# Kernel tuning notes

Measured on AMD Instinct MI355X. Metric: run time of the kernel, lower is better.

Reference implementation:

```python
import jax, jax.numpy as jnp
import numpy as np

B, S, H = 1, 1024, 2048
NH, HD = 16, 128
E, K, FI, SFI = 8, 2, 1408, 2816
EPS = 1e-6
THETA = 10000.0


def setup_inputs() -> dict:
    key = jax.random.key(0)
    ks = jax.random.split(key, 14)
    sc = 0.02
    return {
        "hidden_states": jax.random.normal(ks[0], (B, S, H), jnp.float32),
        "ln1_w": jnp.ones((H,), jnp.float32),
        "ln2_w": jnp.ones((H,), jnp.float32),
        "wq": jax.random.normal(ks[1], (H, H), jnp.float32) * sc,
        "wk": jax.random.normal(ks[2], (H, H), jnp.float32) * sc,
        "wv": jax.random.normal(ks[3], (H, H), jnp.float32) * sc,
        "wo": jax.random.normal(ks[4], (H, H), jnp.float32) * sc,
        "gate_w": jax.random.normal(ks[5], (E, H), jnp.float32) * sc,
        "expert_gate": jax.random.normal(ks[6], (E, FI, H), jnp.float32) * sc,
        "expert_up": jax.random.normal(ks[7], (E, FI, H), jnp.float32) * sc,
        "expert_down": jax.random.normal(ks[8], (E, H, FI), jnp.float32) * sc,
        "shared_gate": jax.random.normal(ks[9], (SFI, H), jnp.float32) * sc,
        "shared_up": jax.random.normal(ks[10], (SFI, H), jnp.float32) * sc,
        "shared_down": jax.random.normal(ks[11], (H, SFI), jnp.float32) * sc,
    }


def _rmsnorm(x, w):
    v = jnp.mean(x * x, axis=-1, keepdims=True)
    return x * jax.lax.rsqrt(v + EPS) * w


def _rotate_half(x):
    x1, x2 = x[..., : HD // 2], x[..., HD // 2 :]
    return jnp.concatenate((-x2, x1), axis=-1)


def _rope_cos_sin():
    inv_freq = 1.0 / (THETA ** (jnp.arange(0, HD, 2, dtype=jnp.float32) / HD))
    t = jnp.arange(S, dtype=jnp.float32)
    freqs = t[:, None] * inv_freq[None, :]          # [S, HD//2]
    emb = jnp.concatenate((freqs, freqs), axis=-1)  # [S, HD]
    return jnp.cos(emb)[None, None], jnp.sin(emb)[None, None]  # [1,1,S,HD]


def _decoder_layer(hidden_states, ln1_w, ln2_w, wq, wk, wv, wo, gate_w,
                   expert_gate, expert_up, expert_down,
                   shared_gate, shared_up, shared_down):
    # ---- self-attention ----
    residual = hidden_states
    h = _rmsnorm(hidden_states, ln1_w)
    q = (h @ wq.T).reshape(B, S, NH, HD).transpose(0, 2, 1, 3)  # [B,NH,S,HD]
    k = (h @ wk.T).reshape(B, S, NH, HD).transpose(0, 2, 1, 3)
    v = (h @ wv.T).reshape(B, S, NH, HD).transpose(0, 2, 1, 3)
    cos, sin = _rope_cos_sin()
    q = q * cos + _rotate_half(q) * sin
    k = k * cos + _rotate_half(k) * sin
    scores = jnp.einsum('bhqd,bhkd->bhqk', q, k) / jnp.sqrt(jnp.float32(HD))
    causal = jnp.tril(jnp.ones((S, S), bool))
    scores = jnp.where(causal[None, None], scores, jnp.finfo(jnp.float32).min)
    probs = jax.nn.softmax(scores, axis=-1)
    attn = jnp.einsum('bhqk,bhkd->bhqd', probs, v)
    attn = attn.transpose(0, 2, 1, 3).reshape(B, S, H)
    x = residual + attn @ wo.T

    # ---- MoE MLP ----
    residual = x
    h2 = _rmsnorm(x, ln2_w)
    flat = h2.reshape(-1, H)                       # [N,H], N=B*S
    n_tok = flat.shape[0]
    logits = flat @ gate_w.T                       # [N,E]
    gate_scores = jax.nn.softmax(logits, axis=-1)
    topk_w, topk_idx = jax.lax.top_k(gate_scores, K)
    topk_w = topk_w / (jnp.sum(topk_w, axis=-1, keepdims=True) + 1e-20)
    # dense combine weights [N,E] (zero for unrouted experts)
    combine = jnp.zeros((n_tok, E), flat.dtype).at[
        jnp.arange(n_tok)[:, None], topk_idx].add(topk_w)
    # SwiGLU per expert, dense over all experts, then weighted combine
    g = jnp.einsum('nh,efh->enf', flat, expert_gate)   # [E,N,FI]
    u = jnp.einsum('nh,efh->enf', flat, expert_up)
    act = jax.nn.silu(g) * u
    eo = jnp.einsum('enf,ehf->enh', act, expert_down)  # [E,N,H]
    routed = jnp.einsum('enh,ne->nh', eo, combine)
    # shared experts (always on)
    shared = (jax.nn.silu(flat @ shared_gate.T) * (flat @ shared_up.T)) @ shared_down.T
    return residual + (routed + shared).reshape(B, S, H)


def reference(hidden_states, ln1_w, ln2_w, wq, wk, wv, wo, gate_w,
              expert_gate, expert_up, expert_down,
              shared_gate, shared_up, shared_down):
    return _decoder_layer(hidden_states, ln1_w, ln2_w, wq, wk, wv, wo, gate_w,
                          expert_gate, expert_up, expert_down,
                          shared_gate, shared_up, shared_down)
```

## Files before the change

### kernel.cpp

```cpp
#include <hip/hip_runtime.h>
#include <hip/hip_bf16.h>


#define DI __device__ __forceinline__

typedef __attribute__((ext_vector_type(8))) short short8;
typedef __attribute__((ext_vector_type(4))) float f32x4;
using u16 = unsigned short;

struct alignas(8) U16x4 { u16 x, y, z, w; };

DI u16 f2bf(float f) {
  unsigned u = __float_as_uint(f);
  u += 0x7fffu + ((u >> 16) & 1u);
  return (u16)(u >> 16);
}
DI float bf2f(u16 h) { return __uint_as_float(((unsigned)h) << 16); }
DI unsigned pack2(float f0, float f1) {
  unsigned a = __float_as_uint(f0) + 0x8000u;
  unsigned b = __float_as_uint(f1) + 0x8000u;
  return (a >> 16) | (b & 0xffff0000u);
}

DI void gload16(const void* g, void* l) {
  __builtin_amdgcn_global_load_lds((const __attribute__((address_space(1))) void*)g,
                                   (__attribute__((address_space(3))) void*)l, 16, 0, 0);
}


__global__ __launch_bounds__(256) void k_ropetab(float* __restrict__ tab) {
  int idx = blockIdx.x * 256 + threadIdx.x;
  int s = idx >> 6, i = idx & 63;
  double inv = pow(10000.0, -(double)(2 * i) / 128.0);
  double ang = (double)s * inv;
  tab[idx * 2 + 0] = (float)cos(ang);
  tab[idx * 2 + 1] = (float)sin(ang);
}

__global__ __launch_bounds__(256) void k_rmsnorm(const float* __restrict__ in,
                                                 const float* __restrict__ w,
                                                 float* __restrict__ outf,
                                                 u16* __restrict__ outh,
                                                 u16* __restrict__ outl) {
  const int row = blockIdx.x, t = threadIdx.x;
  const float* x = in + (size_t)row * 2048;
  float4 a = *(const float4*)&x[t * 4];
  float4 b = *(const float4*)&x[1024 + t * 4];
  float ss = a.x * a.x + a.y * a.y + a.z * a.z + a.w * a.w +
             b.x * b.x + b.y * b.y + b.z * b.z + b.w * b.w;
#pragma unroll
  for (int off = 32; off; off >>= 1) ss += __shfl_xor(ss, off);
  __shared__ float red[4];
  if ((t & 63) == 0) red[t >> 6] = ss;
  __syncthreads();
  float total = red[0] + red[1] + red[2] + red[3];
  float r = 1.0f / sqrtf(total * (1.0f / 2048.0f) + 1e-6f);
  float4 wa = *(const float4*)&w[t * 4];
  float4 wb = *(const float4*)&w[1024 + t * 4];
  float va[8] = {a.x * r * wa.x, a.y * r * wa.y, a.z * r * wa.z, a.w * r * wa.w,
                 b.x * r * wb.x, b.y * r * wb.y, b.z * r * wb.z, b.w * r * wb.w};
  if (outf) {
    *(float4*)&outf[(size_t)row * 2048 + t * 4] = make_float4(va[0], va[1], va[2], va[3]);
    *(float4*)&outf[(size_t)row * 2048 + 1024 + t * 4] = make_float4(va[4], va[5], va[6], va[7]);
  }
  if (outh) {
    U16x4 ha{f2bf(va[0]), f2bf(va[1]), f2bf(va[2]), f2bf(va[3])};
    U16x4 hb{f2bf(va[4]), f2bf(va[5]), f2bf(va[6]), f2bf(va[7])};
    *(U16x4*)&outh[(size_t)row * 2048 + t * 4] = ha;
    *(U16x4*)&outh[(size_t)row * 2048 + 1024 + t * 4] = hb;
    if (outl) {
      U16x4 la{f2bf(va[0] - bf2f(ha.x)), f2bf(va[1] - bf2f(ha.y)),
               f2bf(va[2] - bf2f(ha.z)), f2bf(va[3] - bf2f(ha.w))};
      U16x4 lb{f2bf(va[4] - bf2f(hb.x)), f2bf(va[5] - bf2f(hb.y)),
               f2bf(va[6] - bf2f(hb.z)), f2bf(va[7] - bf2f(hb.w))};
      *(U16x4*)&outl[(size_t)row * 2048 + t * 4] = la;
      *(U16x4*)&outl[(size_t)row * 2048 + 1024 + t * 4] = lb;
    }
  }
}

__global__ __launch_bounds__(256) void k_splitf4(
    const float* __restrict__ s0, const float* __restrict__ s1,
    const float* __restrict__ s2, const float* __restrict__ s3,
    u16* __restrict__ h0, u16* __restrict__ h1, u16* __restrict__ h2,
    u16* __restrict__ h3, u16* __restrict__ l0, u16* __restrict__ l1,
    u16* __restrict__ l2, u16* __restrict__ l3) {
  const int which = blockIdx.x >> 12;
  const int idx = ((blockIdx.x & 4095) * 256 + threadIdx.x) * 4;
  const float* src = (which == 0) ? s0 : (which == 1) ? s1 : (which == 2) ? s2 : s3;
  u16* dh = (which == 0) ? h0 : (which == 1) ? h1 : (which == 2) ? h2 : h3;
  u16* dl = (which == 0) ? l0 : (which == 1) ? l1 : (which == 2) ? l2 : l3;
  float4 v = *(const float4*)&src[idx];
  U16x4 h{f2bf(v.x), f2bf(v.y), f2bf(v.z), f2bf(v.w)};
  U16x4 l{f2bf(v.x - bf2f(h.x)), f2bf(v.y - bf2f(h.y)),
          f2bf(v.z - bf2f(h.z)), f2bf(v.w - bf2f(h.w))};
  *(U16x4*)&dh[idx] = h;
  *(U16x4*)&dl[idx] = l;
}

__global__ __launch_bounds__(256) void k_rope(float* __restrict__ q, float* __restrict__ k,
                                              const float* __restrict__ tab) {
  int idx = blockIdx.x * 256 + threadIdx.x;
  int s = idx >> 10, rem = idx & 1023;
  int h = rem >> 6, i = rem & 63;
  size_t base = (size_t)s * 2048 + h * 128 + i;
  float c = tab[(s * 64 + i) * 2 + 0];
  float sn = tab[(s * 64 + i) * 2 + 1];
  const float qs = 0.08838834764831845f;
  float q1 = q[base], q2 = q[base + 64];
  q[base] = (q1 * c - q2 * sn) * qs;
  q[base + 64] = (q2 * c + q1 * sn) * qs;
  float k1 = k[base], k2 = k[base + 64];
  k[base] = k1 * c - k2 * sn;
  k[base + 64] = k2 * c + k1 * sn;
}

__global__ __launch_bounds__(256) void k_splitkv(
    const float* __restrict__ qf, const float* __restrict__ kf,
    const float* __restrict__ vf,
    u16* __restrict__ Qh, u16* __restrict__ Ql,
    u16* __restrict__ Kh, u16* __restrict__ Kl,
    u16* __restrict__ Vth, u16* __restrict__ Vtl) {
  int idx = (blockIdx.x * 256 + threadIdx.x) * 4;
  int s = idx >> 11, c = idx & 2047;
  float4 q4 = *(const float4*)&qf[idx];
  U16x4 qh{f2bf(q4.x), f2bf(q4.y), f2bf(q4.z), f2bf(q4.w)};
  U16x4 ql{f2bf(q4.x - bf2f(qh.x)), f2bf(q4.y - bf2f(qh.y)),
           f2bf(q4.z - bf2f(qh.z)), f2bf(q4.w - bf2f(qh.w))};
  *(U16x4*)&Qh[idx] = qh; *(U16x4*)&Ql[idx] = ql;
  float4 k4 = *(const float4*)&kf[idx];
  U16x4 kh{f2bf(k4.x), f2bf(k4.y), f2bf(k4.z), f2bf(k4.w)};
  U16x4 kl{f2bf(k4.x - bf2f(kh.x)), f2bf(k4.y - bf2f(kh.y)),
           f2bf(k4.z - bf2f(kh.z)), f2bf(k4.w - bf2f(kh.w))};
  *(U16x4*)&Kh[idx] = kh; *(U16x4*)&Kl[idx] = kl;
  float4 v4 = *(const float4*)&vf[idx];
  float vv[4] = {v4.x, v4.y, v4.z, v4.w};
#pragma unroll
  for (int i = 0; i < 4; ++i) {
    u16 hv = f2bf(vv[i]);
    u16 lv = f2bf(vv[i] - bf2f(hv));
    Vth[(size_t)(c + i) * 1024 + s] = hv;
    Vtl[(size_t)(c + i) * 1024 + s] = lv;
  }
}

DI void stage_kv(const u16* __restrict__ Khg, const u16* __restrict__ Klg,
                 const u16* __restrict__ Vhg, const u16* __restrict__ Vlg,
                 u16* lsKh, u16* lsKl, u16* lsVh, u16* lsVl,
                 int kvb, int hh, int wv, int lane) {
#pragma unroll
  for (int it = 0; it < 4; ++it) {
    const int ebase = it * 2048 + wv * 512;
    const int eo = ebase + lane * 8;
    {
      const int rr = eo >> 7, cg = (eo >> 3) & 15;
      const size_t src = (size_t)(kvb + rr) * 2048 + hh * 128 + ((cg ^ (rr & 7)) << 3);
      gload16(Khg + src, lsKh + ebase);
      gload16(Klg + src, lsKl + ebase);
    }
    {
      const int rr = eo >> 6, cg = (eo >> 3) & 7;
      const size_t src = (size_t)(hh * 128 + rr) * 1024 + kvb + ((cg ^ (rr & 7)) << 3);
      gload16(Vhg + src, lsVh + ebase);
      gload16(Vlg + src, lsVl + ebase);
    }
  }
}

__global__ __launch_bounds__(256) void k_attn_tile(
    const u16* __restrict__ Qh, const u16* __restrict__ Ql,
    const u16* __restrict__ Khg, const u16* __restrict__ Klg,
    const u16* __restrict__ Vhg, const u16* __restrict__ Vlg,
    u16* __restrict__ atth, u16* __restrict__ attl) {
  __shared__ u16 lsKh[2][8192], lsKl[2][8192], lsVh[2][8192], lsVl[2][8192];
  __shared__ u16 Plh[4][16][72], Pll[4][16][72];
  const int hh = blockIdx.y;
  const int qb = blockIdx.x * 64;
  const int tid = threadIdx.x, lane = tid & 63, wv = tid >> 6;
  const int l15 = lane & 15, grp = lane >> 4;
  u16(*plh)[72] = Plh[wv];
  u16(*pll)[72] = Pll[wv];
  const int q_glob = qb + wv * 16 + l15;
  const int tend = blockIdx.x + 1;

  short8 qfh[4], qfl[4];
  const size_t qbase = (size_t)q_glob * 2048 + hh * 128;
#pragma unroll
  for (int c = 0; c < 4; ++c) {
    qfh[c] = *(const short8*)&Qh[qbase + c * 32 + grp * 8];
    qfl[c] = *(const short8*)&Ql[qbase + c * 32 + grp * 8];
  }
  f32x4 oacc[8];
#pragma unroll
  for (int dc = 0; dc < 8; ++dc) oacc[dc] = 0.f;
  float m_run = -1e30f, l_run = 0.f;

  int cur = 0;
  stage_kv(Khg, Klg, Vhg, Vlg, lsKh[0], lsKl[0], lsVh[0], lsVl[0], 0, hh, wv, lane);
  __syncthreads();

  for (int kt = 0; kt < tend; ++kt) {
    const int kvb = kt * 64;
    if (kt + 1 < tend)
      stage_kv(Khg, Klg, Vhg, Vlg, lsKh[cur ^ 1], lsKl[cur ^ 1], lsVh[cur ^ 1],
               lsVl[cur ^ 1], kvb + 64, hh, wv, lane);
    const u16* kh = lsKh[cur];
    const u16* kl = lsKl[cur];
    const u16* vh = lsVh[cur];
    const u16* vl = lsVl[cur];

    f32x4 s4[4];
#pragma unroll
    for (int sub = 0; sub < 4; ++sub) {
      f32x4 a = {0.f, 0.f, 0.f, 0.f};
      const int kr = sub * 16 + l15;
      const int sw = kr & 7;
#pragma unroll
      for (int c = 0; c < 4; ++c) {
        const int off = kr * 128 + ((((c << 2) | grp) ^ sw) << 3);
        short8 khf = *(const short8*)&kh[off];
        short8 klf = *(const short8*)&kl[off];
        a = __builtin_amdgcn_mfma_f32_16x16x32_bf16(khf, qfh[c], a, 0, 0, 0);
        a = __builtin_amdgcn_mfma_f32_16x16x32_bf16(klf, qfh[c], a, 0, 0, 0);
        a = __builtin_amdgcn_mfma_f32_16x16x32_bf16(khf, qfl[c], a, 0, 0, 0);
      }
      s4[sub] = a;
    }
    if (kt == tend - 1) {
#pragma unroll
      for (int sub = 0; sub < 4; ++sub)
#pragma unroll
        for (int r = 0; r < 4; ++r) {
          int kv = kvb + sub * 16 + grp * 4 + r;
          if (kv > q_glob) s4[sub][r] = -1e30f;
        }
    }
    float tmax = s4[0][0];
#pragma unroll
    for (int sub = 0; sub < 4; ++sub)
#pragma unroll
      for (int r = 0; r < 4; ++r) tmax = fmaxf(tmax, s4[sub][r]);
    tmax = fmaxf(tmax, __shfl_xor(tmax, 16));
    tmax = fmaxf(tmax, __shfl_xor(tmax, 32));
    float mnew = fmaxf(m_run, tmax);
    float scale = expf(m_run - mnew);
    float p[16], lsum = 0.f;
#pragma unroll
    for (int sub = 0; sub < 4; ++sub)
#pragma unroll
      for (int r = 0; r < 4; ++r) {
        float pe = expf(s4[sub][r] - mnew);
        p[sub * 4 + r] = pe;
        lsum += pe;
      }
    lsum += __shfl_xor(lsum, 16);
    lsum += __shfl_xor(lsum, 32);
    l_run = l_run * scale + lsum;
    m_run = mnew;
#pragma unroll
    for (int dc = 0; dc < 8; ++dc) oacc[dc] *= scale;
#pragma unroll
    for (int sub = 0; sub < 4; ++sub)
#pragma unroll
      for (int rp = 0; rp < 2; ++rp) {
        int i0 = sub * 4 + rp * 2;
        u16 h0 = f2bf(p[i0]), h1 = f2bf(p[i0 + 1]);
        u16 lo0 = f2bf(p[i0] - bf2f(h0)), lo1 = f2bf(p[i0 + 1] - bf2f(h1));
        int kvoff = sub * 16 + grp * 4 + rp * 2;
        *(unsigned*)&plh[l15][kvoff] = (unsigned)h0 | ((unsigned)h1 << 16);
        *(unsigned*)&pll[l15][kvoff] = (unsigned)lo0 | ((unsigned)lo1 << 16);
      }
    short8 phf[2], plf[2];
#pragma unroll
    for (int ks = 0; ks < 2; ++ks) {
      phf[ks] = *(const short8*)&plh[l15][ks * 32 + grp * 8];
      plf[ks] = *(const short8*)&pll[l15][ks * 32 + grp * 8];
    }
#pragma unroll
    for (int dc = 0; dc < 8; ++dc) {
      const int dr = dc * 16 + l15;
      const int sw = dr & 7;
      f32x4 acc = oacc[dc];
#pragma unroll
      for (int ks = 0; ks < 2; ++ks) {
        const int voff = dr * 64 + ((((ks << 2) | grp) ^ sw) << 3);
        short8 vhf = *(const short8*)&vh[voff];
        short8 vlf = *(const short8*)&vl[voff];
        acc = __builtin_amdgcn_mfma_f32_16x16x32_bf16(vhf, phf[ks], acc, 0, 0, 0);
        acc = __builtin_amdgcn_mfma_f32_16x16x32_bf16(vlf, phf[ks], acc, 0, 0, 0);
        acc = __builtin_amdgcn_mfma_f32_16x16x32_bf16(vhf, plf[ks], acc, 0, 0, 0);
      }
      oacc[dc] = acc;
    }
    __syncthreads();
    cur ^= 1;
  }
  float inv = 1.0f / l_run;
#pragma unroll
  for (int dc = 0; dc < 8; ++dc)
#pragma unroll
    for (int rp = 0; rp < 2; ++rp) {
      float v0 = oacc[dc][rp * 2] * inv;
      float v1 = oacc[dc][rp * 2 + 1] * inv;
      u16 h0 = f2bf(v0), h1 = f2bf(v1);
      u16 lo0 = f2bf(v0 - bf2f(h0)), lo1 = f2bf(v1 - bf2f(h1));
      size_t o = (size_t)q_glob * 2048 + hh * 128 + dc * 16 + grp * 4 + rp * 2;
      *(unsigned*)&atth[o] = (unsigned)h0 | ((unsigned)h1 << 16);
      *(unsigned*)&attl[o] = (unsigned)lo0 | ((unsigned)lo1 << 16);
    }
}

__global__ __launch_bounds__(256) void k_router(const float* __restrict__ h2f,
                                                const float* __restrict__ gw,
                                                int2* __restrict__ tidx,
                                                float2* __restrict__ twgt) {
  const int tok = blockIdx.x;
  const float* hrow = h2f + (size_t)tok * 2048;
  float part[8];
#pragma unroll
  for (int e = 0; e < 8; ++e) part[e] = 0.f;
  for (int j = 0; j < 8; ++j) {
    int p = j * 256 + threadIdx.x;
    float hv = hrow[p];
#pragma unroll
    for (int e = 0; e < 8; ++e) part[e] += hv * gw[e * 2048 + p];
  }
#pragma unroll
  for (int e = 0; e < 8; ++e)
#pragma unroll
    for (int off = 32; off; off >>= 1) part[e] += __shfl_xor(part[e], off);
  __shared__ float red[4][8];
  int wv = threadIdx.x >> 6, lane = threadIdx.x & 63;
  if (lane == 0) {
#pragma unroll
    for (int e = 0; e < 8; ++e) red[wv][e] = part[e];
  }
  __syncthreads();
  if (threadIdx.x == 0) {
    float lg[8];
#pragma unroll
    for (int e = 0; e < 8; ++e) lg[e] = red[0][e] + red[1][e] + red[2][e] + red[3][e];
    float m = lg[0];
#pragma unroll
    for (int e = 1; e < 8; ++e) m = fmaxf(m, lg[e]);
    float ex[8], s = 0.f;
#pragma unroll
    for (int e = 0; e < 8; ++e) { ex[e] = expf(lg[e] - m); s += ex[e]; }
#pragma unroll
    for (int e = 0; e < 8; ++e) ex[e] /= s;
    int i1 = 0;
#pragma unroll
    for (int e = 1; e < 8; ++e) if (ex[e] > ex[i1]) i1 = e;
    int i2 = (i1 == 0) ? 1 : 0;
#pragma unroll
    for (int e = 0; e < 8; ++e) if (e != i1 && ex[e] > ex[i2]) i2 = e;
    float s2 = ex[i1] + ex[i2] + 1e-20f;
    tidx[tok] = make_int2(i1, i2);
    twgt[tok] = make_float2(ex[i1] / s2, ex[i2] / s2);
  }
}

__global__ __launch_bounds__(64) void k_scan(const int2* __restrict__ tidx,
                                             const float2* __restrict__ twgt,
                                             int* __restrict__ meta,
                                             int* __restrict__ toklist,
                                             float* __restrict__ slotw,
                                             int* __restrict__ slots) {
  const int lane = threadIdx.x;
  int base = 0;
  for (int e = 0; e < 8; ++e) {
    int cnt = 0;
    for (int c = 0; c < 16; ++c) {
      const int tok = c * 64 + lane;
      int2 my = tidx[tok];
      int f1 = (my.x == e), f2 = (my.y == e);
      int flag = f1 | f2;
      unsigned long long m = __ballot(flag);
      if (flag) {
        float2 w = twgt[tok];
        int rank = (int)__popcll(m & ((1ull << lane) - 1ull));
        int s = base + cnt + rank;
        toklist[s] = tok;
        slotw[s] = f1 ? w.x : w.y;
        slots[tok * 2 + (f1 ? 0 : 1)] = s;
      }
      cnt += (int)__popcll(m);
    }
    if (lane == 0) { meta[e] = base; meta[9 + e] = cnt; }
    const int padded = ((cnt + 127) >> 7) << 7;
    for (int s = cnt + lane; s < padded; s += 64) {
      toklist[base + s] = 0;
      slotw[base + s] = 0.f;
    }
    base += padded;
  }
  if (lane == 0) meta[8] = base;
}


DI void stageA_bf16(const u16* __restrict__ A, size_t lda, int row0, int k0,
                    u16* lsA, int tid) {
  const int lane = tid & 63, wv = tid >> 6;
#pragma unroll
  for (int it = 0; it < 2; ++it) {
    const int ebase = it * 2048 + wv * 512;
    const int eo = ebase + lane * 8;
    const int rr = eo >> 5, cc = eo & 31;
    gload16(A + (size_t)(row0 + rr) * lda + k0 + cc, lsA + ebase);
  }
}

__global__ __launch_bounds__(256) void k_gemm_bf16split(
    const u16* __restrict__ Ah, const u16* __restrict__ Al,
    const u16* __restrict__ Bh0, const u16* __restrict__ Bl0,
    const u16* __restrict__ Bh1, const u16* __restrict__ Bl1,
    const u16* __restrict__ Bh2, const u16* __restrict__ Bl2,
    float* __restrict__ C0, float* __restrict__ C1, float* __restrict__ C2,
    const float* __restrict__ resid) {
  __shared__ u16 lsAh[4096], lsAl[4096], lsBh[2048], lsBl[2048];
  const int z = blockIdx.z;
  const u16* Bh = (z == 0) ? Bh0 : (z == 1) ? Bh1 : Bh2;
  const u16* Bl = (z == 0) ? Bl0 : (z == 1) ? Bl1 : Bl2;
  float* Cm = (z == 0) ? C0 : (z == 1) ? C1 : C2;
  const int tid = threadIdx.x, lane = tid & 63, wv = tid >> 6;
  const int wr = (wv >> 1) * 64, wc = (wv & 1) * 32;
  const int fr = lane & 15, fg = lane >> 4;
  const int row0 = blockIdx.x * 128, col0 = blockIdx.y * 64;
  f32x4 acc[4][2];
#pragma unroll
  for (int i = 0; i < 4; ++i)
#pragma unroll
    for (int j = 0; j < 2; ++j) acc[i][j] = 0.f;

  for (int kt = 0; kt < 64; ++kt) {
    const int k0 = kt * 32;
    stageA_bf16(Ah, 2048, row0, k0, lsAh, tid);
    stageA_bf16(Al, 2048, row0, k0, lsAl, tid);
    {
      const int ebase = wv * 512;
      const int eo = ebase + lane * 8;
      const int rr = eo >> 5, cc = eo & 31;
      const size_t src = (size_t)(col0 + rr) * 2048 + k0 + cc;
      gload16(Bh + src, lsBh + ebase);
      gload16(Bl + src, lsBl + ebase);
    }
    __syncthreads();
    short8 ah[4], al[4], bh[2], bl[2];
#pragma unroll
    for (int mi = 0; mi < 4; ++mi) {
      const int off = (wr + mi * 16 + fr) * 32 + fg * 8;
      ah[mi] = *(const short8*)&lsAh[off];
      al[mi] = *(const short8*)&lsAl[off];
    }
#pragma unroll
    for (int ni = 0; ni < 2; ++ni) {
      const int off = (wc + ni * 16 + fr) * 32 + fg * 8;
      bh[ni] = *(const short8*)&lsBh[off];
      bl[ni] = *(const short8*)&lsBl[off];
    }
#pragma unroll
    for (int mi = 0; mi < 4; ++mi)
#pragma unroll
      for (int ni = 0; ni < 2; ++ni) {
        f32x4 c = acc[mi][ni];
        c = __builtin_amdgcn_mfma_f32_16x16x32_bf16(al[mi], bh[ni], c, 0, 0, 0);
        c = __builtin_amdgcn_mfma_f32_16x16x32_bf16(ah[mi], bl[ni], c, 0, 0, 0);
        c = __builtin_amdgcn_mfma_f32_16x16x32_bf16(ah[mi], bh[ni], c, 0, 0, 0);
        acc[mi][ni] = c;
      }
    __syncthreads();
  }
  const bool hasres = (resid != nullptr);
#pragma unroll
  for (int mi = 0; mi < 4; ++mi)
#pragma unroll
    for (int ni = 0; ni < 2; ++ni)
#pragma unroll
      for (int qq = 0; qq < 4; ++qq) {
        const int row = row0 + wr + mi * 16 + fg * 4 + qq;
        const int col = col0 + wc + ni * 16 + fr;
        float val = acc[mi][ni][qq];
        if (hasres) val += resid[(size_t)row * 2048 + col];
        Cm[(size_t)row * 2048 + col] = val;
      }
}

DI int tile_to_expert(const int* meta, int t) {
  int e = 0;
  while (e < 7 && t >= (meta[e + 1] >> 7)) ++e;
  return e;
}

__global__ __launch_bounds__(256) void k_dual_all(
    const u16* __restrict__ h2b, const float* __restrict__ eg,
    const float* __restrict__ eu, const float* __restrict__ sg,
    const float* __restrict__ su, const int* __restrict__ meta,
    const int* __restrict__ toklist, const float* __restrict__ slotw,
    u16* __restrict__ act, u16* __restrict__ acts) {
  const int wid = blockIdx.x;
  const bool isShared = wid >= 528;
  __shared__ int toks[128];
  __shared__ u16 lsA[4096], lsG[2048], lsU[2048];
  const int tid = threadIdx.x, lane = tid & 63, wv = tid >> 6;
  const int wr = (wv >> 1) * 64, wc = (wv & 1) * 32;
  const int fr = lane & 15, fg = lane >> 4;

  int n0, off_e = 0, cnt_e = 0, rtile = 0;
  const float *Bg, *Bu;
  if (isShared) {
    const int b2 = wid - 528;
    rtile = b2 / 44;
    n0 = (b2 % 44) * 64;
    Bg = sg;
    Bu = su;
    if (tid < 128) toks[tid] = rtile * 128 + tid;
  } else {
    const int t = wid / 22;
    if (t >= (meta[8] >> 7)) return;
    n0 = (wid % 22) * 64;
    const int e = tile_to_expert(meta, t);
    off_e = meta[e];
    cnt_e = meta[9 + e];
    rtile = t - (off_e >> 7);
    Bg = eg + (size_t)e * 1408 * 2048;
    Bu = eu + (size_t)e * 1408 * 2048;
    if (tid < 128) toks[tid] = toklist[off_e + rtile * 128 + tid] & 1023;
  }
  f32x4 ag[4][2], au[4][2];
#pragma unroll
  for (int i = 0; i < 4; ++i)
#pragma unroll
    for (int j = 0; j < 2; ++j) { ag[i][j] = 0.f; au[i][j] = 0.f; }
  __syncthreads();

  const int ebase0 = wv * 512, ebase1 = 2048 + wv * 512;
  const int eoA0 = ebase0 + lane * 8, eoA1 = ebase1 + lane * 8;
  const u16* aS0 = h2b + (size_t)toks[eoA0 >> 5] * 2048 + (eoA0 & 31);
  const u16* aS1 = h2b + (size_t)toks[eoA1 >> 5] * 2048 + (eoA1 & 31);
  const int eoB0 = tid * 4, eoB1 = (256 + tid) * 4;
  const float* gB0 = Bg + (size_t)(n0 + (eoB0 >> 5)) * 2048 + (eoB0 & 31);
  const float* gB1 = Bg + (size_t)(n0 + (eoB1 >> 5)) * 2048 + (eoB1 & 31);
  const float* uB0 = Bu + (size_t)(n0 + (eoB0 >> 5)) * 2048 + (eoB0 & 31);
  const float* uB1 = Bu + (size_t)(n0 + (eoB1 >> 5)) * 2048 + (eoB1 & 31);

  for (int kt = 0; kt < 64; ++kt) {
    const int k0 = kt * 32;
    gload16(aS0 + k0, lsA + ebase0);
    gload16(aS1 + k0, lsA + ebase1);
    float4 g0 = *(const float4*)(gB0 + k0);
    float4 g1 = *(const float4*)(gB1 + k0);
    float4 u0 = *(const float4*)(uB0 + k0);
    float4 u1 = *(const float4*)(uB1 + k0);
    *(unsigned*)&lsG[eoB0] = pack2(g0.x, g0.y);
    *(unsigned*)&lsG[eoB0 + 2] = pack2(g0.z, g0.w);
    *(unsigned*)&lsG[eoB1] = pack2(g1.x, g1.y);
    *(unsigned*)&lsG[eoB1 + 2] = pack2(g1.z, g1.w);
    *(unsigned*)&lsU[eoB0] = pack2(u0.x, u0.y);
    *(unsigned*)&lsU[eoB0 + 2] = pack2(u0.z, u0.w);
    *(unsigned*)&lsU[eoB1] = pack2(u1.x, u1.y);
    *(unsigned*)&lsU[eoB1 + 2] = pack2(u1.z, u1.w);
    __syncthreads();
    short8 af[4], gf[2], uf[2];
#pragma unroll
    for (int mi = 0; mi < 4; ++mi)
      af[mi] = *(const short8*)&lsA[(wr + mi * 16 + fr) * 32 + fg * 8];
#pragma unroll
    for (int ni = 0; ni < 2; ++ni) {
      const int off = (wc + ni * 16 + fr) * 32 + fg * 8;
      gf[ni] = *(const short8*)&lsG[off];
      uf[ni] = *(const short8*)&lsU[off];
    }
#pragma unroll
    for (int mi = 0; mi < 4; ++mi)
#pragma unroll
      for (int ni = 0; ni < 2; ++ni) {
        ag[mi][ni] = __builtin_amdgcn_mfma_f32_16x16x32_bf16(af[mi], gf[ni], ag[mi][ni], 0, 0, 0);
        au[mi][ni] = __builtin_amdgcn_mfma_f32_16x16x32_bf16(af[mi], uf[ni], au[mi][ni], 0, 0, 0);
      }
    __syncthreads();
  }
#pragma unroll
  for (int mi = 0; mi < 4; ++mi)
#pragma unroll
    for (int ni = 0; ni < 2; ++ni)
#pragma unroll
      for (int qq = 0; qq < 4; ++qq) {
        const int r = wr + mi * 16 + fg * 4 + qq;
        const int col = n0 + wc + ni * 16 + fr;
        float g = ag[mi][ni][qq], u = au[mi][ni][qq];
        float a = g / (1.0f + expf(-g)) * u;
        if (isShared) {
          acts[(size_t)(rtile * 128 + r) * 2816 + col] = f2bf(a);
        } else {
          const int rowInE = rtile * 128 + r;
          if (rowInE < cnt_e)
            act[(size_t)(off_e + rowInE) * 1408 + col] = f2bf(a * slotw[off_e + rowInE]);
        }
      }
}

__global__ __launch_bounds__(256) void k_down_all(
    const u16* __restrict__ act, const float* __restrict__ ed,
    const u16* __restrict__ acts, const float* __restrict__ sd,
    const int* __restrict__ meta, float* __restrict__ dwn,
    float* __restrict__ shd) {
  __shared__ u16 lsA[4096], lsB[4096];
  const int wid = blockIdx.x;
  const int tid = threadIdx.x, lane = tid & 63, wv = tid >> 6;
  const int fr = lane & 15, fg = lane >> 4;
  const int ebase0 = wv * 512, ebase1 = 2048 + wv * 512;
  const int eoA0 = ebase0 + lane * 8, eoA1 = ebase1 + lane * 8;
  if (wid < 384) {
    const int t = wid >> 4;
    if (t >= (meta[8] >> 7)) return;
    const int col0 = (wid & 15) * 128;
    const int e = tile_to_expert(meta, t);
    const int off_e = meta[e];
    const int rtile = t - (off_e >> 7);
    const int wr = (wv >> 1) * 64, wc = (wv & 1) * 64;
    const u16* Ab = act + (size_t)off_e * 1408;
    const float* Bb = ed + (size_t)e * 2048 * 1408;
    const u16* aS0 = Ab + (size_t)(rtile * 128 + (eoA0 >> 5)) * 1408 + (eoA0 & 31);
    const u16* aS1 = Ab + (size_t)(rtile * 128 + (eoA1 >> 5)) * 1408 + (eoA1 & 31);
    const float* bB[4];
    int eoB[4];
#pragma unroll
    for (int j = 0; j < 4; ++j) {
      eoB[j] = (j * 256 + tid) * 4;
      bB[j] = Bb + (size_t)(col0 + (eoB[j] >> 5)) * 1408 + (eoB[j] & 31);
    }
    f32x4 acc[4][4];
#pragma unroll
    for (int i = 0; i < 4; ++i)
#pragma unroll
      for (int j = 0; j < 4; ++j) acc[i][j] = 0.f;
    for (int kt = 0; kt < 44; ++kt) {
      const int k0 = kt * 32;
      gload16(aS0 + k0, lsA + ebase0);
      gload16(aS1 + k0, lsA + ebase1);
      float4 bp[4];
#pragma unroll
      for (int j = 0; j < 4; ++j) bp[j] = *(const float4*)(bB[j] + k0);
#pragma unroll
      for (int j = 0; j < 4; ++j) {
        *(unsigned*)&lsB[eoB[j]] = pack2(bp[j].x, bp[j].y);
        *(unsigned*)&lsB[eoB[j] + 2] = pack2(bp[j].z, bp[j].w);
      }
      __syncthreads();
      short8 af[4], bf_[4];
#pragma unroll
      for (int mi = 0; mi < 4; ++mi)
        af[mi] = *(const short8*)&lsA[(wr + mi * 16 + fr) * 32 + fg * 8];
#pragma unroll
      for (int ni = 0; ni < 4; ++ni)
        bf_[ni] = *(const short8*)&lsB[(wc + ni * 16 + fr) * 32 + fg * 8];
#pragma unroll
      for (int mi = 0; mi < 4; ++mi)
#pragma unroll
        for (int ni = 0; ni < 4; ++ni)
          acc[mi][ni] = __builtin_amdgcn_mfma_f32_16x16x32_bf16(af[mi], bf_[ni], acc[mi][ni], 0, 0, 0);
      __syncthreads();
    }
#pragma unroll
    for (int mi = 0; mi < 4; ++mi)
#pragma unroll
      for (int ni = 0; ni < 4; ++ni)
#pragma unroll
        for (int qq = 0; qq < 4; ++qq) {
          const int r = wr + mi * 16 + fg * 4 + qq;
          const int col = col0 + wc + ni * 16 + fr;
          dwn[(size_t)(off_e + rtile * 128 + r) * 2048 + col] = acc[mi][ni][qq];
        }
  } else {
    const int b2 = wid - 384;
    const int row0 = (b2 >> 5) * 128;
    const int col0 = (b2 & 31) * 64;
    const int wr = (wv >> 1) * 64, wc = (wv & 1) * 32;
    const u16* aS0 = acts + (size_t)(row0 + (eoA0 >> 5)) * 2816 + (eoA0 & 31);
    const u16* aS1 = acts + (size_t)(row0 + (eoA1 >> 5)) * 2816 + (eoA1 & 31);
    const float* bB[2];
    int eoB[2];
#pragma unroll
    for (int j = 0; j < 2; ++j) {
      eoB[j] = (j * 256 + tid) * 4;
      bB[j] = sd + (size_t)(col0 + (eoB[j] >> 5)) * 2816 + (eoB[j] & 31);
    }
    f32x4 acc[4][2];
#pragma unroll
    for (int i = 0; i < 4; ++i)
#pragma unroll
      for (int j = 0; j < 2; ++j) acc[i][j] = 0.f;
    for (int kt = 0; kt < 88; ++kt) {
      const int k0 = kt * 32;
      gload16(aS0 + k0, lsA + ebase0);
      gload16(aS1 + k0, lsA + ebase1);
      float4 bp[2];
#pragma unroll
      for (int j = 0; j < 2; ++j) bp[j] = *(const float4*)(bB[j] + k0);
#pragma unroll
      for (int j = 0; j < 2; ++j) {
        *(unsigned*)&lsB[eoB[j]] = pack2(bp[j].x, bp[j].y);
        *(unsigned*)&lsB[eoB[j] + 2] = pack2(bp[j].z, bp[j].w);
      }
      __syncthreads();
      short8 af[4], bf_[2];
#pragma unroll
      for (int mi = 0; mi < 4; ++mi)
        af[mi] = *(const short8*)&lsA[(wr + mi * 16 + fr) * 32 + fg * 8];
#pragma unroll
      for (int ni = 0; ni < 2; ++ni)
        bf_[ni] = *(const short8*)&lsB[(wc + ni * 16 + fr) * 32 + fg * 8];
#pragma unroll
      for (int mi = 0; mi < 4; ++mi)
#pragma unroll
        for (int ni = 0; ni < 2; ++ni)
          acc[mi][ni] = __builtin_amdgcn_mfma_f32_16x16x32_bf16(af[mi], bf_[ni], acc[mi][ni], 0, 0, 0);
      __syncthreads();
    }
#pragma unroll
    for (int mi = 0; mi < 4; ++mi)
#pragma unroll
      for (int ni = 0; ni < 2; ++ni)
#pragma unroll
        for (int qq = 0; qq < 4; ++qq) {
          const int row = row0 + wr + mi * 16 + fg * 4 + qq;
          const int col = col0 + wc + ni * 16 + fr;
          shd[(size_t)row * 2048 + col] = acc[mi][ni][qq];
        }
  }
}

__global__ __launch_bounds__(256) void k_combine(
    const float* __restrict__ shd, const float* __restrict__ x,
    const float* __restrict__ dwn, const int* __restrict__ slots,
    float* __restrict__ outp) {
  const int i4 = (blockIdx.x * 256 + threadIdx.x) * 4;
  const int row = i4 >> 11, col = i4 & 2047;
  const int s0 = slots[row * 2], s1 = slots[row * 2 + 1];
  float4 a = *(const float4*)&shd[i4];
  float4 b = *(const float4*)&x[i4];
  float4 c = *(const float4*)&dwn[(size_t)s0 * 2048 + col];
  float4 d = *(const float4*)&dwn[(size_t)s1 * 2048 + col];
  float4 o;
  o.x = a.x + b.x + c.x + d.x;
  o.y = a.y + b.y + c.y + d.y;
  o.z = a.z + b.z + c.z + d.z;
  o.w = a.w + b.w + c.w + d.w;
  *(float4*)&outp[i4] = o;
}


extern "C" void kernel_launch(void* const* d_in, const int* in_sizes, int n_in,
                              void* d_out, int out_size, void* d_ws, size_t ws_size,
                              hipStream_t stream) {
  (void)in_sizes; (void)n_in; (void)out_size; (void)ws_size;
  const float* hidden = (const float*)d_in[0];
  const float* ln1 = (const float*)d_in[1];
  const float* ln2 = (const float*)d_in[2];
  const float* wq = (const float*)d_in[3];
  const float* wk = (const float*)d_in[4];
  const float* wvw = (const float*)d_in[5];
  const float* wo = (const float*)d_in[6];
  const float* gw = (const float*)d_in[7];
  const float* eg = (const float*)d_in[8];
  const float* eu = (const float*)d_in[9];
  const float* ed = (const float*)d_in[10];
  const float* sg = (const float*)d_in[11];
  const float* su = (const float*)d_in[12];
  const float* sd = (const float*)d_in[13];
  float* out = (float*)d_out;
  char* ws = (char*)d_ws;

  const size_t KB = 1ull << 10, MB = 1ull << 20;
  float* tab = (float*)(ws + 0);
  int2* tidx = (int2*)(ws + 512 * KB);
  float2* twgt = (float2*)(ws + 520 * KB);
  int* meta = (int*)(ws + 528 * KB);
  int* tokl = (int*)(ws + 532 * KB);
  float* slw = (float*)(ws + 544 * KB);
  int* slots = (int*)(ws + 556 * KB);
  u16* hnh = (u16*)(ws + 1 * MB);
  u16* hnl = (u16*)(ws + 5 * MB);
  u16* wqh = (u16*)(ws + 9 * MB);
  u16* wql = (u16*)(ws + 17 * MB);
  u16* wkh = (u16*)(ws + 25 * MB);
  u16* wkl = (u16*)(ws + 33 * MB);
  u16* wvh = (u16*)(ws + 41 * MB);
  u16* wvl = (u16*)(ws + 49 * MB);
  u16* woh = (u16*)(ws + 57 * MB);
  u16* wol = (u16*)(ws + 65 * MB);
  float* qf = (float*)(ws + 73 * MB);
  float* kf = (float*)(ws + 81 * MB);
  float* vf = (float*)(ws + 89 * MB);
  u16* Qh = (u16*)(ws + 9 * MB);
  u16* Ql = (u16*)(ws + 13 * MB);
  u16* Kh = (u16*)(ws + 17 * MB);
  u16* Kl = (u16*)(ws + 21 * MB);
  u16* Vth = (u16*)(ws + 25 * MB);
  u16* Vtl = (u16*)(ws + 29 * MB);
  u16* atth = (u16*)(ws + 33 * MB);
  u16* attl = (u16*)(ws + 37 * MB);
  float* xf = (float*)(ws + 41 * MB);
  float* h2f = (float*)(ws + 49 * MB);
  u16* h2b = (u16*)(ws + 1 * MB);
  u16* act = (u16*)(ws + 73 * MB);
  u16* acts = (u16*)(ws + 82 * MB);
  float* dwn = (float*)(ws + 9 * MB);
  float* shd = (float*)(ws + 33 * MB);

  k_ropetab<<<256, 256, 0, stream>>>(tab);
  k_rmsnorm<<<1024, 256, 0, stream>>>(hidden, ln1, nullptr, hnh, hnl);
  k_splitf4<<<16384, 256, 0, stream>>>(wq, wk, wvw, wo, wqh, wkh, wvh, woh,
                                       wql, wkl, wvl, wol);
  k_gemm_bf16split<<<dim3(8, 32, 3), 256, 0, stream>>>(
      hnh, hnl, wqh, wql, wkh, wkl, wvh, wvl, qf, kf, vf, nullptr);
  k_rope<<<4096, 256, 0, stream>>>(qf, kf, tab);
  k_splitkv<<<2048, 256, 0, stream>>>(qf, kf, vf, Qh, Ql, Kh, Kl, Vth, Vtl);
  k_attn_tile<<<dim3(16, 16), 256, 0, stream>>>(Qh, Ql, Kh, Kl, Vth, Vtl, atth, attl);
  k_gemm_bf16split<<<dim3(8, 32, 1), 256, 0, stream>>>(
      atth, attl, woh, wol, woh, wol, woh, wol, xf, xf, xf, hidden);
  k_rmsnorm<<<1024, 256, 0, stream>>>(xf, ln2, h2f, h2b, nullptr);
  k_router<<<1024, 256, 0, stream>>>(h2f, gw, tidx, twgt);
  k_scan<<<1, 64, 0, stream>>>(tidx, twgt, meta, tokl, slw, slots);
  k_dual_all<<<880, 256, 0, stream>>>(h2b, eg, eu, sg, su, meta, tokl, slw, act, acts);
  k_down_all<<<640, 256, 0, stream>>>(act, ed, acts, sd, meta, dwn, shd);
  k_combine<<<2048, 256, 0, stream>>>(shd, xf, dwn, slots, out);
}
```

Before: 546.7 us.

## Double K-tile depth to 64 with XOR-swizzled LDS layout in GEMM kernels

All four GEMM kernels (attention projections, expert gate/up, expert/shared down) now stage a 64-wide K slice per iteration instead of 32. This halves the number of loop iterations and __syncthreads barriers. Shared-memory tiles use a row-XOR swizzle on 8-element groups, applied to both the global-to-LDS copy addresses and the fragment reads, to reduce LDS bank conflicts. LDS use per block doubles, which may lower occupancy.

Result: no change. 554.3 us (+1.4%).

```diff
diff --git a/kernel.cpp b/kernel.cpp
--- a/kernel.cpp
+++ b/kernel.cpp
@@ -398,18 +398,6 @@
 }
 
 
-DI void stageA_bf16(const u16* __restrict__ A, size_t lda, int row0, int k0,
-                    u16* lsA, int tid) {
-  const int lane = tid & 63, wv = tid >> 6;
-#pragma unroll
-  for (int it = 0; it < 2; ++it) {
-    const int ebase = it * 2048 + wv * 512;
-    const int eo = ebase + lane * 8;
-    const int rr = eo >> 5, cc = eo & 31;
-    gload16(A + (size_t)(row0 + rr) * lda + k0 + cc, lsA + ebase);
-  }
-}
-
 __global__ __launch_bounds__(256) void k_gemm_bf16split(
     const u16* __restrict__ Ah, const u16* __restrict__ Al,
     const u16* __restrict__ Bh0, const u16* __restrict__ Bl0,
@@ -417,7 +405,7 @@
     const u16* __restrict__ Bh2, const u16* __restrict__ Bl2,
     float* __restrict__ C0, float* __restrict__ C1, float* __restrict__ C2,
     const float* __restrict__ resid) {
-  __shared__ u16 lsAh[4096], lsAl[4096], lsBh[2048], lsBl[2048];
+  __shared__ u16 lsAh[8192], lsAl[8192], lsBh[4096], lsBl[4096];
   const int z = blockIdx.z;
   const u16* Bh = (z == 0) ? Bh0 : (z == 1) ? Bh1 : Bh2;
   const u16* Bl = (z == 0) ? Bl0 : (z == 1) ? Bl1 : Bl2;
@@ -432,42 +420,63 @@
 #pragma unroll
     for (int j = 0; j < 2; ++j) acc[i][j] = 0.f;
 
-  for (int kt = 0; kt < 64; ++kt) {
-    const int k0 = kt * 32;
-    stageA_bf16(Ah, 2048, row0, k0, lsAh, tid);
-    stageA_bf16(Al, 2048, row0, k0, lsAl, tid);
-    {
-      const int ebase = wv * 512;
-      const int eo = ebase + lane * 8;
-      const int rr = eo >> 5, cc = eo & 31;
-      const size_t src = (size_t)(col0 + rr) * 2048 + k0 + cc;
-      gload16(Bh + src, lsBh + ebase);
-      gload16(Bl + src, lsBl + ebase);
+  size_t aoff[4], boff[2];
+#pragma unroll
+  for (int it = 0; it < 4; ++it) {
+    const int eo = it * 2048 + wv * 512 + lane * 8;
+    const int r = eo >> 6, g = (eo >> 3) & 7;
+    aoff[it] = (size_t)(row0 + r) * 2048 + ((g ^ (r & 7)) << 3);
+  }
+#pragma unroll
+  for (int it = 0; it < 2; ++it) {
+    const int eo = it * 2048 + wv * 512 + lane * 8;
+    const int r = eo >> 6, g = (eo >> 3) & 7;
+    boff[it] = (size_t)(col0 + r) * 2048 + ((g ^ (r & 7)) << 3);
+  }
+
+  for (int kt = 0; kt < 32; ++kt) {
+    const int k0 = kt * 64;
+#pragma unroll
+    for (int it = 0; it < 4; ++it) {
+      const int ebase = it * 2048 + wv * 512;
+      gload16(Ah + aoff[it] + k0, lsAh + ebase);
+      gload16(Al + aoff[it] + k0, lsAl + ebase);
+    }
+#pragma unroll
+    for (int it = 0; it < 2; ++it) {
+      const int ebase = it * 2048 + wv * 512;
+      gload16(Bh + boff[it] + k0, lsBh + ebase);
+      gload16(Bl + boff[it] + k0, lsBl + ebase);
     }
     __syncthreads();
-    short8 ah[4], al[4], bh[2], bl[2];
-#pragma unroll
-    for (int mi = 0; mi < 4; ++mi) {
-      const int off = (wr + mi * 16 + fr) * 32 + fg * 8;
-      ah[mi] = *(const short8*)&lsAh[off];
-      al[mi] = *(const short8*)&lsAl[off];
-    }
-#pragma unroll
-    for (int ni = 0; ni < 2; ++ni) {
-      const int off = (wc + ni * 16 + fr) * 32 + fg * 8;
-      bh[ni] = *(const short8*)&lsBh[off];
-      bl[ni] = *(const short8*)&lsBl[off];
-    }
-#pragma unroll
-    for (int mi = 0; mi < 4; ++mi)
+#pragma unroll
+    for (int kk = 0; kk < 2; ++kk) {
+      short8 ah[4], al[4], bh[2], bl[2];
+#pragma unroll
+      for (int mi = 0; mi < 4; ++mi) {
+        const int row = wr + mi * 16 + fr;
+        const int off = row * 64 + ((kk * 32 + fg * 8) ^ ((row & 7) << 3));
+        ah[mi] = *(const short8*)&lsAh[off];
+        al[mi] = *(const short8*)&lsAl[off];
+      }
 #pragma unroll
       for (int ni = 0; ni < 2; ++ni) {
-        f32x4 c = acc[mi][ni];
-        c = __builtin_amdgcn_mfma_f32_16x16x32_bf16(al[mi], bh[ni], c, 0, 0, 0);
-        c = __builtin_amdgcn_mfma_f32_16x16x32_bf16(ah[mi], bl[ni], c, 0, 0, 0);
-        c = __builtin_amdgcn_mfma_f32_16x16x32_bf16(ah[mi], bh[ni], c, 0, 0, 0);
-        acc[mi][ni] = c;
-      }
+        const int row = wc + ni * 16 + fr;
+        const int off = row * 64 + ((kk * 32 + fg * 8) ^ ((row & 7) << 3));
+        bh[ni] = *(const short8*)&lsBh[off];
+        bl[ni] = *(const short8*)&lsBl[off];
+      }
+#pragma unroll
+      for (int mi = 0; mi < 4; ++mi)
+#pragma unroll
+        for (int ni = 0; ni < 2; ++ni) {
+          f32x4 c = acc[mi][ni];
+          c = __builtin_amdgcn_mfma_f32_16x16x32_bf16(al[mi], bh[ni], c, 0, 0, 0);
+          c = __builtin_amdgcn_mfma_f32_16x16x32_bf16(ah[mi], bl[ni], c, 0, 0, 0);
+          c = __builtin_amdgcn_mfma_f32_16x16x32_bf16(ah[mi], bh[ni], c, 0, 0, 0);
+          acc[mi][ni] = c;
+        }
+    }
     __syncthreads();
   }
   const bool hasres = (resid != nullptr);
@@ -500,7 +509,7 @@
   const int wid = blockIdx.x;
   const bool isShared = wid >= 528;
   __shared__ int toks[128];
-  __shared__ u16 lsA[4096], lsG[2048], lsU[2048];
+  __shared__ u16 lsA[8192], lsG[4096], lsU[4096];
   const int tid = threadIdx.x, lane = tid & 63, wv = tid >> 6;
   const int wr = (wv >> 1) * 64, wc = (wv & 1) * 32;
   const int fr = lane & 15, fg = lane >> 4;
@@ -533,50 +542,62 @@
     for (int j = 0; j < 2; ++j) { ag[i][j] = 0.f; au[i][j] = 0.f; }
   __syncthreads();
 
-  const int ebase0 = wv * 512, ebase1 = 2048 + wv * 512;
-  const int eoA0 = ebase0 + lane * 8, eoA1 = ebase1 + lane * 8;
-  const u16* aS0 = h2b + (size_t)toks[eoA0 >> 5] * 2048 + (eoA0 & 31);
-  const u16* aS1 = h2b + (size_t)toks[eoA1 >> 5] * 2048 + (eoA1 & 31);
-  const int eoB0 = tid * 4, eoB1 = (256 + tid) * 4;
-  const float* gB0 = Bg + (size_t)(n0 + (eoB0 >> 5)) * 2048 + (eoB0 & 31);
-  const float* gB1 = Bg + (size_t)(n0 + (eoB1 >> 5)) * 2048 + (eoB1 & 31);
-  const float* uB0 = Bu + (size_t)(n0 + (eoB0 >> 5)) * 2048 + (eoB0 & 31);
-  const float* uB1 = Bu + (size_t)(n0 + (eoB1 >> 5)) * 2048 + (eoB1 & 31);
-
-  for (int kt = 0; kt < 64; ++kt) {
-    const int k0 = kt * 32;
-    gload16(aS0 + k0, lsA + ebase0);
-    gload16(aS1 + k0, lsA + ebase1);
-    float4 g0 = *(const float4*)(gB0 + k0);
-    float4 g1 = *(const float4*)(gB1 + k0);
-    float4 u0 = *(const float4*)(uB0 + k0);
-    float4 u1 = *(const float4*)(uB1 + k0);
-    *(unsigned*)&lsG[eoB0] = pack2(g0.x, g0.y);
-    *(unsigned*)&lsG[eoB0 + 2] = pack2(g0.z, g0.w);
-    *(unsigned*)&lsG[eoB1] = pack2(g1.x, g1.y);
-    *(unsigned*)&lsG[eoB1 + 2] = pack2(g1.z, g1.w);
-    *(unsigned*)&lsU[eoB0] = pack2(u0.x, u0.y);
-    *(unsigned*)&lsU[eoB0 + 2] = pack2(u0.z, u0.w);
-    *(unsigned*)&lsU[eoB1] = pack2(u1.x, u1.y);
-    *(unsigned*)&lsU[eoB1 + 2] = pack2(u1.z, u1.w);
+  const u16* aS[4];
+#pragma unroll
+  for (int it = 0; it < 4; ++it) {
+    const int eo = it * 2048 + wv * 512 + lane * 8;
+    const int r = eo >> 6, g = (eo >> 3) & 7;
+    aS[it] = h2b + (size_t)toks[r] * 2048 + ((g ^ (r & 7)) << 3);
+  }
+  const float *gB[4], *uB[4];
+  int sB[4];
+#pragma unroll
+  for (int j = 0; j < 4; ++j) {
+    const int eo = (j * 256 + tid) * 4;
+    const int row = eo >> 6, colu = eo & 63;
+    sB[j] = row * 64 + (colu ^ ((row & 7) << 3));
+    gB[j] = Bg + (size_t)(n0 + row) * 2048 + colu;
+    uB[j] = Bu + (size_t)(n0 + row) * 2048 + colu;
+  }
+
+  for (int kt = 0; kt < 32; ++kt) {
+    const int k0 = kt * 64;
+#pragma unroll
+    for (int it = 0; it < 4; ++it)
+      gload16(aS[it] + k0, lsA + it * 2048 + wv * 512);
+#pragma unroll
+    for (int j = 0; j < 4; ++j) {
+      float4 g = *(const float4*)(gB[j] + k0);
+      float4 u = *(const float4*)(uB[j] + k0);
+      *(unsigned*)&lsG[sB[j]] = pack2(g.x, g.y);
+      *(unsigned*)&lsG[sB[j] + 2] = pack2(g.z, g.w);
+      *(unsigned*)&lsU[sB[j]] = pack2(u.x, u.y);
+      *(unsigned*)&lsU[sB[j] + 2] = pack2(u.z, u.w);
+    }
     __syncthreads();
-    short8 af[4], gf[2], uf[2];
-#pragma unroll
-    for (int mi = 0; mi < 4; ++mi)
-      af[mi] = *(const short8*)&lsA[(wr + mi * 16 + fr) * 32 + fg * 8];
-#pragma unroll
-    for (int ni = 0; ni < 2; ++ni) {
-      const int off = (wc + ni * 16 + fr) * 32 + fg * 8;
-      gf[ni] = *(const short8*)&lsG[off];
-      uf[ni] = *(const short8*)&lsU[off];
-    }
-#pragma unroll
-    for (int mi = 0; mi < 4; ++mi)
+#pragma unroll
+    for (int kk = 0; kk < 2; ++kk) {
+      short8 af[4], gf[2], uf[2];
+#pragma unroll
+      for (int mi = 0; mi < 4; ++mi) {
+        const int row = wr + mi * 16 + fr;
+        af[mi] = *(const short8*)&lsA[row * 64 + ((kk * 32 + fg * 8) ^ ((row & 7) << 3))];
+      }
 #pragma unroll
       for (int ni = 0; ni < 2; ++ni) {
-        ag[mi][ni] = __builtin_amdgcn_mfma_f32_16x16x32_bf16(af[mi], gf[ni], ag[mi][ni], 0, 0, 0);
-        au[mi][ni] = __builtin_amdgcn_mfma_f32_16x16x32_bf16(af[mi], uf[ni], au[mi][ni], 0, 0, 0);
-      }
+        const int row = wc + ni * 16 + fr;
+        const int off = row * 64 + ((kk * 32 + fg * 8) ^ ((row & 7) << 3));
+        gf[ni] = *(const short8*)&lsG[off];
+        uf[ni] = *(const short8*)&lsU[off];
+      }
+#pragma unroll
+      for (int mi = 0; mi < 4; ++mi)
+#pragma unroll
+        for (int ni = 0; ni < 2; ++ni) {
+          ag[mi][ni] = __builtin_amdgcn_mfma_f32_16x16x32_bf16(af[mi], gf[ni], ag[mi][ni], 0, 0, 0);
+          au[mi][ni] = __builtin_amdgcn_mfma_f32_16x16x32_bf16(af[mi], uf[ni], au[mi][ni], 0, 0, 0);
+        }
+    }
     __syncthreads();
   }
 #pragma unroll
@@ -604,12 +625,10 @@
     const u16* __restrict__ acts, const float* __restrict__ sd,
     const int* __restrict__ meta, float* __restrict__ dwn,
     float* __restrict__ shd) {
-  __shared__ u16 lsA[4096], lsB[4096];
+  __shared__ u16 lsA[8192], lsB[8192];
   const int wid = blockIdx.x;
   const int tid = threadIdx.x, lane = tid & 63, wv = tid >> 6;
   const int fr = lane & 15, fg = lane >> 4;
-  const int ebase0 = wv * 512, ebase1 = 2048 + wv * 512;
-  const int eoA0 = ebase0 + lane * 8, eoA1 = ebase1 + lane * 8;
   if (wid < 384) {
     const int t = wid >> 4;
     if (t >= (meta[8] >> 7)) return;
@@ -620,45 +639,58 @@
     const int wr = (wv >> 1) * 64, wc = (wv & 1) * 64;
     const u16* Ab = act + (size_t)off_e * 1408;
     const float* Bb = ed + (size_t)e * 2048 * 1408;
-    const u16* aS0 = Ab + (size_t)(rtile * 128 + (eoA0 >> 5)) * 1408 + (eoA0 & 31);
-    const u16* aS1 = Ab + (size_t)(rtile * 128 + (eoA1 >> 5)) * 1408 + (eoA1 & 31);
-    const float* bB[4];
-    int eoB[4];
-#pragma unroll
-    for (int j = 0; j < 4; ++j) {
-      eoB[j] = (j * 256 + tid) * 4;
-      bB[j] = Bb + (size_t)(col0 + (eoB[j] >> 5)) * 1408 + (eoB[j] & 31);
+    const u16* aS[4];
+#pragma unroll
+    for (int it = 0; it < 4; ++it) {
+      const int eo = it * 2048 + wv * 512 + lane * 8;
+      const int r = eo >> 6, g = (eo >> 3) & 7;
+      aS[it] = Ab + (size_t)(rtile * 128 + r) * 1408 + ((g ^ (r & 7)) << 3);
+    }
+    const float* bB[8];
+    int sB[8];
+#pragma unroll
+    for (int j = 0; j < 8; ++j) {
+      const int eo = (j * 256 + tid) * 4;
+      const int row = eo >> 6, colu = eo & 63;
+      sB[j] = row * 64 + (colu ^ ((row & 7) << 3));
+      bB[j] = Bb + (size_t)(col0 + row) * 1408 + colu;
     }
     f32x4 acc[4][4];
 #pragma unroll
     for (int i = 0; i < 4; ++i)
 #pragma unroll
       for (int j = 0; j < 4; ++j) acc[i][j] = 0.f;
-    for (int kt = 0; kt < 44; ++kt) {
-      const int k0 = kt * 32;
-      gload16(aS0 + k0, lsA + ebase0);
-      gload16(aS1 + k0, lsA + ebase1);
-      float4 bp[4];
-#pragma unroll
-      for (int j = 0; j < 4; ++j) bp[j] = *(const float4*)(bB[j] + k0);
-#pragma unroll
-      for (int j = 0; j < 4; ++j) {
-        *(unsigned*)&lsB[eoB[j]] = pack2(bp[j].x, bp[j].y);
-        *(unsigned*)&lsB[eoB[j] + 2] = pack2(bp[j].z, bp[j].w);
+    for (int kt = 0; kt < 22; ++kt) {
+      const int k0 = kt * 64;
+#pragma unroll
+      for (int it = 0; it < 4; ++it)
+        gload16(aS[it] + k0, lsA + it * 2048 + wv * 512);
+#pragma unroll
+      for (int j = 0; j < 8; ++j) {
+        float4 b = *(const float4*)(bB[j] + k0);
+        *(unsigned*)&lsB[sB[j]] = pack2(b.x, b.y);
+        *(unsigned*)&lsB[sB[j] + 2] = pack2(b.z, b.w);
       }
       __syncthreads();
-      short8 af[4], bf_[4];
-#pragma unroll
-      for (int mi = 0; mi < 4; ++mi)
-        af[mi] = *(const short8*)&lsA[(wr + mi * 16 + fr) * 32 + fg * 8];
-#pragma unroll
-      for (int ni = 0; ni < 4; ++ni)
-        bf_[ni] = *(const short8*)&lsB[(wc + ni * 16 + fr) * 32 + fg * 8];
-#pragma unroll
-      for (int mi = 0; mi < 4; ++mi)
-#pragma unroll
-        for (int ni = 0; ni < 4; ++ni)
-          acc[mi][ni] = __builtin_amdgcn_mfma_f32_16x16x32_bf16(af[mi], bf_[ni], acc[mi][ni], 0, 0, 0);
+#pragma unroll
+      for (int kk = 0; kk < 2; ++kk) {
+        short8 af[4], bf_[4];
+#pragma unroll
+        for (int mi = 0; mi < 4; ++mi) {
+          const int row = wr + mi * 16 + fr;
+          af[mi] = *(const short8*)&lsA[row * 64 + ((kk * 32 + fg * 8) ^ ((row & 7) << 3))];
+        }
+#pragma unroll
+        for (int ni = 0; ni < 4; ++ni) {
+          const int row = wc + ni * 16 + fr;
+          bf_[ni] = *(const short8*)&lsB[row * 64 + ((kk * 32 + fg * 8) ^ ((row & 7) << 3))];
+        }
+#pragma unroll
+        for (int mi = 0; mi < 4; ++mi)
+#pragma unroll
+          for (int ni = 0; ni < 4; ++ni)
+            acc[mi][ni] = __builtin_amdgcn_mfma_f32_16x16x32_bf16(af[mi], bf_[ni], acc[mi][ni], 0, 0, 0);
+      }
       __syncthreads();
     }
 #pragma unroll
@@ -676,45 +708,58 @@
     const int row0 = (b2 >> 5) * 128;
     const int col0 = (b2 & 31) * 64;
     const int wr = (wv >> 1) * 64, wc = (wv & 1) * 32;
-    const u16* aS0 = acts + (size_t)(row0 + (eoA0 >> 5)) * 2816 + (eoA0 & 31);
-    const u16* aS1 = acts + (size_t)(row0 + (eoA1 >> 5)) * 2816 + (eoA1 & 31);
-    const float* bB[2];
-    int eoB[2];
-#pragma unroll
-    for (int j = 0; j < 2; ++j) {
-      eoB[j] = (j * 256 + tid) * 4;
-      bB[j] = sd + (size_t)(col0 + (eoB[j] >> 5)) * 2816 + (eoB[j] & 31);
+    const u16* aS[4];
+#pragma unroll
+    for (int it = 0; it < 4; ++it) {
+      const int eo = it * 2048 + wv * 512 + lane * 8;
+      const int r = eo >> 6, g = (eo >> 3) & 7;
+      aS[it] = acts + (size_t)(row0 + r) * 2816 + ((g ^ (r & 7)) << 3);
+    }
+    const float* bB[4];
+    int sB[4];
+#pragma unroll
+    for (int j = 0; j < 4; ++j) {
+      const int eo = (j * 256 + tid) * 4;
+      const int row = eo >> 6, colu = eo & 63;
+      sB[j] = row * 64 + (colu ^ ((row & 7) << 3));
+      bB[j] = sd + (size_t)(col0 + row) * 2816 + colu;
     }
     f32x4 acc[4][2];
 #pragma unroll
     for (int i = 0; i < 4; ++i)
 #pragma unroll
       for (int j = 0; j < 2; ++j) acc[i][j] = 0.f;
-    for (int kt = 0; kt < 88; ++kt) {
-      const int k0 = kt * 32;
-      gload16(aS0 + k0, lsA + ebase0);
-      gload16(aS1 + k0, lsA + ebase1);
-      float4 bp[2];
-#pragma unroll
-      for (int j = 0; j < 2; ++j) bp[j] = *(const float4*)(bB[j] + k0);
-#pragma unroll
-      for (int j = 0; j < 2; ++j) {
-        *(unsigned*)&lsB[eoB[j]] = pack2(bp[j].x, bp[j].y);
-        *(unsigned*)&lsB[eoB[j] + 2] = pack2(bp[j].z, bp[j].w);
+    for (int kt = 0; kt < 44; ++kt) {
+      const int k0 = kt * 64;
+#pragma unroll
+      for (int it = 0; it < 4; ++it)
+        gload16(aS[it] + k0, lsA + it * 2048 + wv * 512);
+#pragma unroll
+      for (int j = 0; j < 4; ++j) {
+        float4 b = *(const float4*)(bB[j] + k0);
+        *(unsigned*)&lsB[sB[j]] = pack2(b.x, b.y);
+        *(unsigned*)&lsB[sB[j] + 2] = pack2(b.z, b.w);
       }
       __syncthreads();
-      short8 af[4], bf_[2];
-#pragma unroll
-      for (int mi = 0; mi < 4; ++mi)
-        af[mi] = *(const short8*)&lsA[(wr + mi * 16 + fr) * 32 + fg * 8];
-#pragma unroll
-      for (int ni = 0; ni < 2; ++ni)
-        bf_[ni] = *(const short8*)&lsB[(wc + ni * 16 + fr) * 32 + fg * 8];
-#pragma unroll
-      for (int mi = 0; mi < 4; ++mi)
-#pragma unroll
-        for (int ni = 0; ni < 2; ++ni)
-          acc[mi][ni] = __builtin_amdgcn_mfma_f32_16x16x32_bf16(af[mi], bf_[ni], acc[mi][ni], 0, 0, 0);
+#pragma unroll
+      for (int kk = 0; kk < 2; ++kk) {
+        short8 af[4], bf_[2];
+#pragma unroll
+        for (int mi = 0; mi < 4; ++mi) {
+          const int row = wr + mi * 16 + fr;
+          af[mi] = *(const short8*)&lsA[row * 64 + ((kk * 32 + fg * 8) ^ ((row & 7) << 3))];
+        }
+#pragma unroll
+        for (int ni = 0; ni < 2; ++ni) {
+          const int row = wc + ni * 16 + fr;
+          bf_[ni] = *(const short8*)&lsB[row * 64 + ((kk * 32 + fg * 8) ^ ((row & 7) << 3))];
+        }
+#pragma unroll
+        for (int mi = 0; mi < 4; ++mi)
+#pragma unroll
+          for (int ni = 0; ni < 2; ++ni)
+            acc[mi][ni] = __builtin_amdgcn_mfma_f32_16x16x32_bf16(af[mi], bf_[ni], acc[mi][ni], 0, 0, 0);
+      }
       __syncthreads();
     }
 #pragma unroll
```
